# Kernel tuning notes

Hardware: AMD Instinct MI355X
Metric: run time of the kernel (lower is better)

Reference implementation:

```python
import jax, jax.numpy as jnp
import numpy as np

N = 131072
DIMS = [3, 128, 128, 128, 128, 4]

RHO1, RHO2 = 1000.0, 1.225
MU1, MU2 = 1e-3, 1.8e-5
SIGMA, G = 0.0728, 9.81
U_REF, L_REF = 1.0, 1.0


def setup_inputs() -> dict:
    key = jax.random.key(0)
    ks = jax.random.split(key, 3 + 2 * (len(DIMS) - 1))
    inp = {
        "x": jax.random.uniform(ks[0], (N, 1), dtype=jnp.float32),
        "y": jax.random.uniform(ks[1], (N, 1), dtype=jnp.float32),
        "t": jax.random.uniform(ks[2], (N, 1), dtype=jnp.float32),
    }
    for i in range(len(DIMS) - 1):
        fan_in, fan_out = DIMS[i], DIMS[i + 1]
        scale = jnp.sqrt(2.0 / (fan_in + fan_out)).astype(jnp.float32)  # glorot
        inp[f"W{i}"] = jax.random.normal(ks[3 + 2 * i], (fan_in, fan_out), dtype=jnp.float32) * scale
        inp[f"b{i}"] = jax.random.normal(ks[4 + 2 * i], (fan_out,), dtype=jnp.float32) * 0.01
    return inp


def _mlp(pt, params):
    # pt: (3,) -> (4,) tanh MLP
    h = pt
    for W, b in params[:-1]:
        h = jnp.tanh(h @ W + b)
    W, b = params[-1]
    return h @ W + b


def reference(x, y, t, W0, b0, W1, b1, W2, b2, W3, b3, W4, b4):
    params = [(W0, b0), (W1, b1), (W2, b2), (W3, b3), (W4, b4)]
    pts = jnp.concatenate([x, y, t], axis=1)  # [N,3]
    f = lambda p: _mlp(p, params)

    out = jax.vmap(f)(pts)                           # [N,4] -> (u,v,p,a)
    jac = jax.vmap(jax.jacfwd(f))(pts)               # [N,4,3] d out_i / d (x,y,t)_j
    hess = jax.vmap(jax.jacfwd(jax.jacfwd(f)))(pts)  # [N,4,3,3]

    u, v, a = out[:, 0], out[:, 1], out[:, 3]
    u_x, u_y, u_t = jac[:, 0, 0], jac[:, 0, 1], jac[:, 0, 2]
    v_x, v_y, v_t = jac[:, 1, 0], jac[:, 1, 1], jac[:, 1, 2]
    p_x, p_y = jac[:, 2, 0], jac[:, 2, 1]
    a_x, a_y, a_t = jac[:, 3, 0], jac[:, 3, 1], jac[:, 3, 2]
    u_xx, u_yy = hess[:, 0, 0, 0], hess[:, 0, 1, 1]
    v_xx, v_yy = hess[:, 1, 0, 0], hess[:, 1, 1, 1]
    a_xx, a_yy, a_xy = hess[:, 3, 0, 0], hess[:, 3, 1, 1], hess[:, 3, 0, 1]

    mu = MU2 + (MU1 - MU2) * a
    mu_x = (MU1 - MU2) * a_x
    mu_y = (MU1 - MU2) * a_y
    rho = RHO2 + (RHO1 - RHO2) * a

    abs_grad_a = jnp.sqrt(a_x ** 2 + a_y ** 2 + 1e-12)
    curvature = -((a_xx + a_yy) / abs_grad_a
                  - (a_x ** 2 * a_xx + a_y ** 2 * a_yy + 2.0 * a_x * a_y * a_xy) / abs_grad_a ** 3)

    rho_ref = RHO2
    denom = rho_ref * U_REF * L_REF
    one_Re = mu / denom
    one_Re_x = mu_x / denom
    one_Re_y = mu_y / denom
    one_We = SIGMA / (rho_ref * U_REF ** 2 * L_REF)
    one_Fr = G * L_REF / U_REF ** 2

    PDE_m = u_x + v_y
    PDE_a = a_t + u * a_x + v * a_y
    PDE_u = ((u_t + u * u_x + v * u_y) * rho / rho_ref + p_x
             - one_We * curvature * a_x - one_Re * (u_xx + u_yy)
             - 2.0 * one_Re_x * u_x - one_Re_y * (u_y + v_x))
    PDE_v = ((v_t + u * v_x + v * v_y) * rho / rho_ref + p_y
             - one_We * curvature * a_y - rho / rho_ref * one_Fr
             - one_Re * (v_xx + v_yy) - 2.0 * one_Re_y * v_y - one_Re_x * (u_y + v_x))

    return jnp.stack([PDE_m, PDE_u, PDE_v, PDE_a], axis=1)  # [N,4]
```

## Files before the change

### kernel.cpp

```cpp
#include <hip/hip_runtime.h>
#include <cmath>

typedef __attribute__((ext_vector_type(8))) _Float16 f16x8;
typedef __attribute__((ext_vector_type(2))) _Float16 f16x2;
typedef __attribute__((ext_vector_type(4))) float f32x4;
typedef unsigned int u32;

__device__ __forceinline__ float tanh_fast(float z) {
    float e = __builtin_amdgcn_exp2f(z * 2.8853900817779268f);
    return 1.0f - 2.0f * __builtin_amdgcn_rcpf(e + 1.0f);
}

__device__ __forceinline__ float f4c(const float4& v, int i) {
    switch (i) { case 0: return v.x; case 1: return v.y; case 2: return v.z; default: return v.w; }
}

__global__ void prep_w_frags(const float* __restrict__ W1, const float* __restrict__ W2,
                             const float* __restrict__ W3, const float* __restrict__ W4,
                             unsigned short* __restrict__ wsf)
{
    int t = blockIdx.x * blockDim.x + threadIdx.x;
    int l = t >> 14;
    int rem = t & 16383;
    int k = rem >> 7;
    int j = rem & 127;
    float f;
    if (l == 0)      f = W1[k*128 + j];
    else if (l == 1) f = W2[k*128 + j];
    else if (l == 2) f = W3[k*128 + j];
    else {
        if (j >= 16) return;
        f = (j < 4) ? W4[k*4 + j] : 0.0f;
    }
    _Float16 hf = (_Float16)f;
    unsigned short h16 = __builtin_bit_cast(unsigned short, hf);
    int n = j >> 4, jm = j & 15;
    int kc = k >> 5, half = (k >> 4) & 1, qk = (k >> 2) & 3, e = k & 3;
    int lane = qk*16 + jm, s = half*4 + e;
    size_t idx = (((size_t)l*8 + n)*4 + kc)*512 + (size_t)lane*8 + s;
    wsf[idx] = h16;
}

__global__ __launch_bounds__(256, 4)
void pinn_mfma_kernel(
    const float* __restrict__ gx, const float* __restrict__ gy, const float* __restrict__ gt,
    const float* __restrict__ W0, const float* __restrict__ b0,
    const float* __restrict__ b1, const float* __restrict__ b2, const float* __restrict__ b3,
    const float* __restrict__ b4,
    const unsigned short* __restrict__ wsf,
    float* __restrict__ out, int n)
{
    __shared__ uint4 Sfh[4][7][64];
    __shared__ uint4 Sfl[4][64];

    const int tid  = threadIdx.x;
    const int lane = tid & 63;
    const int wv   = tid >> 6;
    const int q    = lane >> 4;
    const int jm   = lane & 15;
    const int gp0  = blockIdx.x * 16;

    auto wfrag = [&](int l, int mt, int kc) -> f16x8 {
        return *reinterpret_cast<const f16x8*>(
            wsf + (((size_t)l*8 + mt)*4 + kc)*512 + (size_t)lane*8);
    };

    int gp = gp0 + jm; if (gp >= n) gp = n - 1;
    const float xv = gx[gp], yv = gy[gp], tv = gt[gp];

    const int j0a = (2*wv + 0)*16 + q*4;
    const int j0b = (2*wv + 1)*16 + q*4;
    float4 w0x[2], w0y[2], w0t[2], b0v[2], bias[3][2];
    w0x[0] = *reinterpret_cast<const float4*>(W0 + j0a);
    w0x[1] = *reinterpret_cast<const float4*>(W0 + j0b);
    w0y[0] = *reinterpret_cast<const float4*>(W0 + 128 + j0a);
    w0y[1] = *reinterpret_cast<const float4*>(W0 + 128 + j0b);
    w0t[0] = *reinterpret_cast<const float4*>(W0 + 256 + j0a);
    w0t[1] = *reinterpret_cast<const float4*>(W0 + 256 + j0b);
    b0v[0] = *reinterpret_cast<const float4*>(b0 + j0a);
    b0v[1] = *reinterpret_cast<const float4*>(b0 + j0b);
    bias[0][0] = *reinterpret_cast<const float4*>(b1 + j0a);
    bias[0][1] = *reinterpret_cast<const float4*>(b1 + j0b);
    bias[1][0] = *reinterpret_cast<const float4*>(b2 + j0a);
    bias[1][1] = *reinterpret_cast<const float4*>(b2 + j0b);
    bias[2][0] = *reinterpret_cast<const float4*>(b3 + j0a);
    bias[2][1] = *reinterpret_cast<const float4*>(b3 + j0b);

    u32 hw[7][4], lw[4];
    float tmp[7];
    auto pack7 = [&](int sidx, const float* o) {
        if ((sidx & 1) == 0) {
            #pragma unroll
            for (int v = 0; v < 7; ++v) tmp[v] = o[v];
        } else {
            const int d = sidx >> 1;
            #pragma unroll
            for (int v = 0; v < 7; ++v) {
                _Float16 h0 = (_Float16)tmp[v];
                _Float16 h1 = (_Float16)o[v];
                f16x2 hp; hp[0] = h0; hp[1] = h1;
                hw[v][d] = __builtin_bit_cast(u32, hp);
                if (v == 0) {
                    float l0 = tmp[0] - (float)h0;
                    float l1 = o[0]   - (float)h1;
                    f16x2 lp; lp[0] = (_Float16)l0; lp[1] = (_Float16)l1;
                    lw[d] = __builtin_bit_cast(u32, lp);
                }
            }
        }
    };
    auto storeFrags = [&]() {
        #pragma unroll
        for (int v = 0; v < 7; ++v)
            Sfh[wv][v][lane] = make_uint4(hw[v][0], hw[v][1], hw[v][2], hw[v][3]);
        Sfl[wv][lane] = make_uint4(lw[0], lw[1], lw[2], lw[3]);
    };

    #pragma unroll
    for (int ms = 0; ms < 2; ++ms) {
        #pragma unroll
        for (int i = 0; i < 4; ++i) {
            const float wx = f4c(w0x[ms], i), wy = f4c(w0y[ms], i), wt = f4c(w0t[ms], i);
            float z = fmaf(xv, wx, fmaf(yv, wy, fmaf(tv, wt, f4c(b0v[ms], i))));
            float s = tanh_fast(z);
            float d = 1.0f - s*s;
            float m2sd = -2.0f * s * d;
            float o[7] = { s, d*wx, d*wy, d*wt, m2sd*wx*wx, m2sd*wy*wy, m2sd*wx*wy };
            pack7(ms*4 + i, o);
        }
    }
    storeFrags();
    __syncthreads();

    #pragma unroll
    for (int l = 0; l < 3; ++l) {
        f16x8 wf[2][4];
        #pragma unroll
        for (int ms = 0; ms < 2; ++ms)
          #pragma unroll
          for (int kc = 0; kc < 4; ++kc)
            wf[ms][kc] = wfrag(l, 2*wv + ms, kc);

        f32x4 acc[7][2];
        #pragma unroll
        for (int v = 0; v < 7; ++v)
          #pragma unroll
          for (int ms = 0; ms < 2; ++ms)
            acc[v][ms] = (f32x4){0.f, 0.f, 0.f, 0.f};

        #pragma unroll
        for (int kc = 0; kc < 4; ++kc) {
          #pragma unroll
          for (int v = 0; v < 7; ++v) {
            f16x8 bh = *reinterpret_cast<const f16x8*>(&Sfh[kc][v][lane]);
            #pragma unroll
            for (int ms = 0; ms < 2; ++ms)
                acc[v][ms] = __builtin_amdgcn_mfma_f32_16x16x32_f16(wf[ms][kc], bh, acc[v][ms], 0, 0, 0);
            if (v == 0) {
                f16x8 bl = *reinterpret_cast<const f16x8*>(&Sfl[kc][lane]);
                #pragma unroll
                for (int ms = 0; ms < 2; ++ms)
                    acc[0][ms] = __builtin_amdgcn_mfma_f32_16x16x32_f16(wf[ms][kc], bl, acc[0][ms], 0, 0, 0);
            }
          }
        }
        __syncthreads();

        #pragma unroll
        for (int ms = 0; ms < 2; ++ms) {
            #pragma unroll
            for (int i = 0; i < 4; ++i) {
                float z   = acc[0][ms][i] + f4c(bias[l][ms], i);
                float zx  = acc[1][ms][i];
                float zy  = acc[2][ms][i];
                float zt  = acc[3][ms][i];
                float zxx = acc[4][ms][i];
                float zyy = acc[5][ms][i];
                float zxy = acc[6][ms][i];
                float s = tanh_fast(z);
                float d = 1.0f - s*s;
                float m2s = -2.0f * s;
                float o[7] = { s, d*zx, d*zy, d*zt,
                               d * fmaf(m2s * zx, zx, zxx),
                               d * fmaf(m2s * zy, zy, zyy),
                               d * fmaf(m2s * zx, zy, zxy) };
                pack7(ms*4 + i, o);
            }
        }
        storeFrags();
        __syncthreads();
    }

    if (wv == 0) {
        f16x8 w4[4];
        #pragma unroll
        for (int kc = 0; kc < 4; ++kc)
            w4[kc] = wfrag(3, 0, kc);

        f32x4 a4[7];
        #pragma unroll
        for (int v = 0; v < 7; ++v) a4[v] = (f32x4){0.f, 0.f, 0.f, 0.f};

        #pragma unroll
        for (int kc = 0; kc < 4; ++kc)
          #pragma unroll
          for (int v = 0; v < 7; ++v) {
            f16x8 bh = *reinterpret_cast<const f16x8*>(&Sfh[kc][v][lane]);
            a4[v] = __builtin_amdgcn_mfma_f32_16x16x32_f16(w4[kc], bh, a4[v], 0, 0, 0);
            if (v == 0) {
                f16x8 bl = *reinterpret_cast<const f16x8*>(&Sfl[kc][lane]);
                a4[0] = __builtin_amdgcn_mfma_f32_16x16x32_f16(w4[kc], bl, a4[0], 0, 0, 0);
            }
          }

        if (q == 0) {
            float r[7][4];
            #pragma unroll
            for (int v = 0; v < 7; ++v) {
                r[v][0] = a4[v][0]; r[v][1] = a4[v][1];
                r[v][2] = a4[v][2]; r[v][3] = a4[v][3];
            }
            const float u  = r[0][0] + b4[0];
            const float v  = r[0][1] + b4[1];
            const float a  = r[0][3] + b4[3];
            const float u_x = r[1][0], u_y = r[2][0], u_t = r[3][0];
            const float v_x = r[1][1], v_y = r[2][1], v_t = r[3][1];
            const float p_x = r[1][2], p_y = r[2][2];
            const float a_x = r[1][3], a_y = r[2][3], a_t = r[3][3];
            const float u_xx = r[4][0], u_yy = r[5][0];
            const float v_xx = r[4][1], v_yy = r[5][1];
            const float a_xx = r[4][3], a_yy = r[5][3], a_xy = r[6][3];

            const float MU1 = 0.001f, MU2 = 1.8e-5f;
            const float RHO1 = 1000.0f, RHO2 = 1.225f;
            const float SIGMA = 0.0728f, GACC = 9.81f;

            const float mu   = MU2 + (MU1 - MU2) * a;
            const float mu_x = (MU1 - MU2) * a_x;
            const float mu_y = (MU1 - MU2) * a_y;
            const float rho  = RHO2 + (RHO1 - RHO2) * a;

            const float abs_grad = sqrtf(a_x*a_x + a_y*a_y + 1e-12f);
            const float ag3 = abs_grad * abs_grad * abs_grad;
            const float curvature =
                -((a_xx + a_yy) / abs_grad
                  - (a_x*a_x*a_xx + a_y*a_y*a_yy + 2.0f*a_x*a_y*a_xy) / ag3);

            const float one_Re   = mu   / RHO2;
            const float one_Re_x = mu_x / RHO2;
            const float one_Re_y = mu_y / RHO2;
            const float one_We   = SIGMA / RHO2;
            const float one_Fr   = GACC;
            const float rr       = rho / RHO2;

            const float PDE_m = u_x + v_y;
            const float PDE_a = a_t + u*a_x + v*a_y;
            const float PDE_u = (u_t + u*u_x + v*u_y) * rr + p_x
                                - one_We * curvature * a_x
                                - one_Re * (u_xx + u_yy)
                                - 2.0f * one_Re_x * u_x
                                - one_Re_y * (u_y + v_x);
            const float PDE_v = (v_t + u*v_x + v*v_y) * rr + p_y
                                - one_We * curvature * a_y
                                - rr * one_Fr
                                - one_Re * (v_xx + v_yy)
                                - 2.0f * one_Re_y * v_y
                                - one_Re_x * (u_y + v_x);

            if (gp0 + jm < n) {
                float4 res; res.x = PDE_m; res.y = PDE_u; res.z = PDE_v; res.w = PDE_a;
                *reinterpret_cast<float4*>(out + (size_t)(gp0 + jm) * 4) = res;
            }
        }
    }
}

extern "C" void kernel_launch(void* const* d_in, const int* in_sizes, int n_in,
                              void* d_out, int out_size, void* d_ws, size_t ws_size,
                              hipStream_t stream)
{
    const float* x  = (const float*)d_in[0];
    const float* y  = (const float*)d_in[1];
    const float* t  = (const float*)d_in[2];
    const float* W0 = (const float*)d_in[3];
    const float* b0 = (const float*)d_in[4];
    const float* W1 = (const float*)d_in[5];
    const float* b1 = (const float*)d_in[6];
    const float* W2 = (const float*)d_in[7];
    const float* b2 = (const float*)d_in[8];
    const float* W3 = (const float*)d_in[9];
    const float* b3 = (const float*)d_in[10];
    const float* W4 = (const float*)d_in[11];
    const float* b4 = (const float*)d_in[12];
    float* out = (float*)d_out;
    unsigned short* wsf = (unsigned short*)d_ws;

    const int n = in_sizes[0];

    prep_w_frags<<<256, 256, 0, stream>>>(W1, W2, W3, W4, wsf);

    const int grid = (n + 15) / 16;
    pinn_mfma_kernel<<<grid, 256, 0, stream>>>(
        x, y, t, W0, b0, b1, b2, b3, b4, wsf, out, n);
}
```

Baseline: 193.2 us.

## Drop fp16 residual split for activations, use packed RTZ convert and own-fragment reuse

Removes the hi/lo fp16 split of the layer value activations, which eliminates one of the eight MFMA groups per k-chunk along with its LDS buffer. Packing now uses the hardware cvt_pkrtz instruction. Each wave reuses its own fragments from registers instead of reading them back from LDS. The occupancy hint rises from 4 to 5 waves per SIMD. Truncation rounding and dropping the residual lower the precision of the primal activations, which may affect accuracy of the PDE residuals.

```diff
diff --git a/kernel.cpp b/kernel.cpp
--- a/kernel.cpp
+++ b/kernel.cpp
@@ -2,7 +2,7 @@
 #include <cmath>
 
 typedef __attribute__((ext_vector_type(8))) _Float16 f16x8;
-typedef __attribute__((ext_vector_type(2))) _Float16 f16x2;
+typedef __attribute__((ext_vector_type(2))) __fp16 fp16x2;
 typedef __attribute__((ext_vector_type(4))) float f32x4;
 typedef unsigned int u32;
 
@@ -13,6 +13,11 @@
 
 __device__ __forceinline__ float f4c(const float4& v, int i) {
     switch (i) { case 0: return v.x; case 1: return v.y; case 2: return v.z; default: return v.w; }
+}
+
+__device__ __forceinline__ u32 pk16(float a, float b) {
+    fp16x2 hp = __builtin_amdgcn_cvt_pkrtz(a, b);
+    return __builtin_bit_cast(u32, hp);
 }
 
 __global__ void prep_w_frags(const float* __restrict__ W1, const float* __restrict__ W2,
@@ -41,7 +46,7 @@
     wsf[idx] = h16;
 }
 
-__global__ __launch_bounds__(256, 4)
+__global__ __launch_bounds__(256, 5)
 void pinn_mfma_kernel(
     const float* __restrict__ gx, const float* __restrict__ gy, const float* __restrict__ gt,
     const float* __restrict__ W0, const float* __restrict__ b0,
@@ -51,7 +56,6 @@
     float* __restrict__ out, int n)
 {
     __shared__ uint4 Sfh[4][7][64];
-    __shared__ uint4 Sfl[4][64];
 
     const int tid  = threadIdx.x;
     const int lane = tid & 63;
@@ -86,7 +90,7 @@
     bias[2][0] = *reinterpret_cast<const float4*>(b3 + j0a);
     bias[2][1] = *reinterpret_cast<const float4*>(b3 + j0b);
 
-    u32 hw[7][4], lw[4];
+    u32 hw[7][4];
     float tmp[7];
     auto pack7 = [&](int sidx, const float* o) {
         if ((sidx & 1) == 0) {
@@ -95,25 +99,17 @@
         } else {
             const int d = sidx >> 1;
             #pragma unroll
-            for (int v = 0; v < 7; ++v) {
-                _Float16 h0 = (_Float16)tmp[v];
-                _Float16 h1 = (_Float16)o[v];
-                f16x2 hp; hp[0] = h0; hp[1] = h1;
-                hw[v][d] = __builtin_bit_cast(u32, hp);
-                if (v == 0) {
-                    float l0 = tmp[0] - (float)h0;
-                    float l1 = o[0]   - (float)h1;
-                    f16x2 lp; lp[0] = (_Float16)l0; lp[1] = (_Float16)l1;
-                    lw[d] = __builtin_bit_cast(u32, lp);
-                }
-            }
+            for (int v = 0; v < 7; ++v)
+                hw[v][d] = pk16(tmp[v], o[v]);
         }
     };
     auto storeFrags = [&]() {
         #pragma unroll
         for (int v = 0; v < 7; ++v)
             Sfh[wv][v][lane] = make_uint4(hw[v][0], hw[v][1], hw[v][2], hw[v][3]);
-        Sfl[wv][lane] = make_uint4(lw[0], lw[1], lw[2], lw[3]);
+    };
+    auto ownFrag = [&](int v) -> f16x8 {
+        return __builtin_bit_cast(f16x8, make_uint4(hw[v][0], hw[v][1], hw[v][2], hw[v][3]));
     };
 
     #pragma unroll
@@ -152,16 +148,11 @@
         for (int kc = 0; kc < 4; ++kc) {
           #pragma unroll
           for (int v = 0; v < 7; ++v) {
-            f16x8 bh = *reinterpret_cast<const f16x8*>(&Sfh[kc][v][lane]);
+            f16x8 bh = (kc == wv) ? ownFrag(v)
+                                  : *reinterpret_cast<const f16x8*>(&Sfh[kc][v][lane]);
             #pragma unroll
             for (int ms = 0; ms < 2; ++ms)
                 acc[v][ms] = __builtin_amdgcn_mfma_f32_16x16x32_f16(wf[ms][kc], bh, acc[v][ms], 0, 0, 0);
-            if (v == 0) {
-                f16x8 bl = *reinterpret_cast<const f16x8*>(&Sfl[kc][lane]);
-                #pragma unroll
-                for (int ms = 0; ms < 2; ++ms)
-                    acc[0][ms] = __builtin_amdgcn_mfma_f32_16x16x32_f16(wf[ms][kc], bl, acc[0][ms], 0, 0, 0);
-            }
           }
         }
         __syncthreads();
@@ -205,12 +196,9 @@
         for (int kc = 0; kc < 4; ++kc)
           #pragma unroll
           for (int v = 0; v < 7; ++v) {
-            f16x8 bh = *reinterpret_cast<const f16x8*>(&Sfh[kc][v][lane]);
+            f16x8 bh = (kc == 0) ? ownFrag(v)
+                                 : *reinterpret_cast<const f16x8*>(&Sfh[kc][v][lane]);
             a4[v] = __builtin_amdgcn_mfma_f32_16x16x32_f16(w4[kc], bh, a4[v], 0, 0, 0);
-            if (v == 0) {
-                f16x8 bl = *reinterpret_cast<const f16x8*>(&Sfl[kc][lane]);
-                a4[0] = __builtin_amdgcn_mfma_f32_16x16x32_f16(w4[kc], bl, a4[0], 0, 0, 0);
-            }
           }
 
         if (q == 0) {
```

New measurement: 647.0 us. +234.8%, slower.
